# Kernel optimization log

Measured on AMD Instinct MI355X. Metric: run time of the kernel, lower is better.

Reference implementation:

```python
import jax, jax.numpy as jnp
import numpy as np

IN_F = 4096
OUT_F = 11008
GROUP_SIZE = 128
NUM_GROUPS = (IN_F + GROUP_SIZE - 1) // GROUP_SIZE  # 32
N_HIGH = int(OUT_F * 0.25)   # 2752
N_LOW = OUT_F - N_HIGH       # 8256
B, S = 2, 2048


def setup_inputs() -> dict:
    key = jax.random.key(0)
    ks = jax.random.split(key, 9)
    x = jax.random.normal(ks[0], (B, S, IN_F), dtype=jnp.float32)
    # INT8 symmetric codes for high-precision columns
    high_prec_weight = jax.random.randint(ks[1], (IN_F, N_HIGH), -128, 128, dtype=jnp.int32)
    # per-group, per-column scales (positive, realistic magnitude)
    high_prec_scales = jax.random.uniform(ks[2], (NUM_GROUPS, N_HIGH), jnp.float32, 1e-4, 2e-2)
    # 4-bit asymmetric codes in [0, 15]
    low_prec_weight = jax.random.randint(ks[3], (IN_F, N_LOW), 0, 16, dtype=jnp.int32)
    low_prec_scales = jax.random.uniform(ks[4], (IN_F, 1), jnp.float32, 1e-4, 2e-2)
    low_prec_scales2 = jax.random.uniform(ks[5], (1, N_LOW), jnp.float32, 0.5, 2.0)
    low_prec_zeros = jnp.round(jax.random.uniform(ks[6], (IN_F, 1), jnp.float32, 0.0, 15.0))
    # inverse column permutation restoring original order
    col_indices_inv = jax.random.permutation(ks[7], OUT_F).astype(jnp.int64)
    bias = jax.random.normal(ks[8], (OUT_F,), dtype=jnp.float32) * 0.02
    return {
        "x": x,
        "high_prec_weight": high_prec_weight,
        "high_prec_scales": high_prec_scales,
        "low_prec_weight": low_prec_weight,
        "low_prec_scales": low_prec_scales,
        "low_prec_scales2": low_prec_scales2,
        "low_prec_zeros": low_prec_zeros,
        "col_indices_inv": col_indices_inv,
        "bias": bias,
    }


def _dequantize(high_w, high_scales, low_w, low_s1, low_s2, low_z, col_inv):
    # High: group-wise symmetric INT8 dequant. K divisible by GROUP_SIZE here (no pad).
    w_high = (high_w.astype(jnp.float32)
              .reshape(NUM_GROUPS, GROUP_SIZE, N_HIGH)
              * high_scales[:, None, :]).reshape(IN_F, N_HIGH)
    # Low: SINQ dual-scale asymmetric dequant: ((q - z) * s1) * s2
    w_low = (low_w.astype(jnp.float32) - low_z) * low_s1 * low_s2
    # Reassemble original column order: W_kn [in_features, out_features]
    w = jnp.concatenate([w_high, w_low], axis=1)[:, col_inv]
    return w


def reference(x, high_prec_weight, high_prec_scales, low_prec_weight,
              low_prec_scales, low_prec_scales2, low_prec_zeros,
              col_indices_inv, bias):
    w_kn = _dequantize(high_prec_weight, high_prec_scales, low_prec_weight,
                       low_prec_scales, low_prec_scales2, low_prec_zeros,
                       col_indices_inv)
    # F.linear(x, W_original) with W_original = w_kn.T  ->  x @ w_kn
    out = jnp.einsum('bsk,kn->bsn', x, w_kn) + bias
    return out
```

## Files before the change

### kernel.cpp

```cpp
#include <hip/hip_runtime.h>
#include <hip/hip_bf16.h>

#define IN_F   4096
#define OUT_F  11008
#define NHIGH  2752
#define NLOW   8256
#define M_TOT  4096

typedef __attribute__((ext_vector_type(8))) short bf16x8;
typedef __attribute__((ext_vector_type(4))) float f32x4;
typedef __attribute__((ext_vector_type(4))) float f32x4v;

__device__ __forceinline__ short f2bf(float f) {
    union { float f; unsigned u; } v; v.f = f;
    unsigned r = (v.u + 0x7fffu + ((v.u >> 16) & 1u)) >> 16;
    return (short)(r & 0xffffu);
}

__device__ __forceinline__ void async16(const void* g, const void* l) {
    __builtin_amdgcn_global_load_lds(
        (const __attribute__((address_space(1))) unsigned int*)g,
        (__attribute__((address_space(3))) unsigned int*)l, 16, 0, 0);
}

__global__ void fwd_perm_kernel(const int* __restrict__ cinv, int* __restrict__ fwd) {
    int n = blockIdx.x * blockDim.x + threadIdx.x;
    if (n < OUT_F) fwd[cinv[n]] = n;
}

__global__ void cvt_x_kernel(const float* __restrict__ x, short* __restrict__ xb) {
    const int nv = (M_TOT * IN_F) / 8;
    for (int i = blockIdx.x * blockDim.x + threadIdx.x; i < nv;
         i += gridDim.x * blockDim.x) {
        const f32x4v* p = (const f32x4v*)(x + (long)i * 8);
        f32x4v a = __builtin_nontemporal_load(p);
        f32x4v b = __builtin_nontemporal_load(p + 1);
        bf16x8 o;
        o[0] = f2bf(a[0]); o[1] = f2bf(a[1]); o[2] = f2bf(a[2]); o[3] = f2bf(a[3]);
        o[4] = f2bf(b[0]); o[5] = f2bf(b[1]); o[6] = f2bf(b[2]); o[7] = f2bf(b[3]);
        *(bf16x8*)(xb + (long)i * 8) = o;
    }
}

__global__ void dequant_kernel(const int* __restrict__ hw, const float* __restrict__ hs,
                               const int* __restrict__ lw, const float* __restrict__ s1,
                               const float* __restrict__ s2, const float* __restrict__ zp,
                               const int* __restrict__ fwd,
                               short* __restrict__ wt) {
    __shared__ short tile[64 * 66];
    const int t  = threadIdx.x;
    const int c0 = blockIdx.x * 64;
    const int k0 = blockIdx.y * 64;
    const int cl = t & 63;
    const int w  = t >> 6;

    if (c0 < NHIGH) {
        const int ci = c0 + cl;
        #pragma unroll
        for (int i = 0; i < 16; ++i) {
            const int kl = w + 4 * i;
            const int k  = k0 + kl;
            int   q   = __builtin_nontemporal_load(&hw[(long)k * NHIGH + ci]);
            float val = (float)q * hs[(k >> 7) * NHIGH + ci];
            tile[cl * 66 + kl] = f2bf(val);
        }
    } else {
        const int ci = c0 - NHIGH + cl;
        const float s2v = s2[ci];
        #pragma unroll
        for (int i = 0; i < 16; ++i) {
            const int kl = w + 4 * i;
            const int k  = k0 + kl;
            int   q   = __builtin_nontemporal_load(&lw[(long)k * NLOW + ci]);
            float val = ((float)q - zp[k]) * s1[k] * s2v;
            tile[cl * 66 + kl] = f2bf(val);
        }
    }
    __syncthreads();
    const int oc = t >> 2;
    const int kq = (t & 3) * 16;
    bf16x8 o0, o1;
    #pragma unroll
    for (int j = 0; j < 8; ++j) {
        o0[j] = tile[oc * 66 + kq + j];
        o1[j] = tile[oc * 66 + kq + 8 + j];
    }
    const int ndst = fwd[c0 + oc];
    short* dst = wt + (long)ndst * IN_F + k0 + kq;
    *(bf16x8*)dst       = o0;
    *(bf16x8*)(dst + 8) = o1;
}

#define BM 256
#define BN 256
#define BK 64
#define KT (IN_F / BK)
#define NTIL (OUT_F / BN)
#define MTIL (M_TOT / BM)
#define NWG2 (NTIL * MTIL)

#define BAR()    __builtin_amdgcn_s_barrier()
#define VMC0()   asm volatile("s_waitcnt vmcnt(0)" ::: "memory")

__global__ __launch_bounds__(512, 2) void gemm_kernel(
    const short* __restrict__ A,
    const short* __restrict__ Bt,
    const float* __restrict__ bias,
    float* __restrict__ C) {
    __shared__ __align__(16) short lds_s[65536];
    char* const lds = (char*)lds_s;

    const int t    = threadIdx.x;
    const int lane = t & 63;
    const int w    = t >> 6;
    const int wr   = w >> 2;
    const int wc   = w & 3;

    const int swz   = (blockIdx.x % 8) * (NWG2 / 8) + blockIdx.x / 8;
    const int sr    = swz / (4 * NTIL);
    const int in_sr = swz % (4 * NTIL);
    const int nb    = in_sr / 4;
    const int mb    = sr * 4 + (in_sr & 3);
    const int m0    = mb * BM;
    const int n0    = nb * BN;

    const int srow = w * 8 + (lane >> 3);
    const int scb  = ((lane & 7) ^ (lane >> 3)) * 16;
    const char* gA0 = (const char*)A  + (long)(m0 + srow) * (IN_F * 2) + scb;
    const char* gB0 = (const char*)Bt + (long)(n0 + srow) * (IN_F * 2) + scb;

    const int rl  = (lane & 15) * 128;
    const int kb0 = ((lane >> 4) * 16) ^ ((lane & 7) << 4);
    const int kb1 = kb0 ^ 64;

#define STAGE(gbase, region_off, h, ktile) do {                                  \
        const char* _g = (gbase) + (long)((h) * 128) * (IN_F * 2) + (ktile) * 128; \
        char* _l = lds + (region_off) + (h) * 16384 + w * 1024;                  \
        async16(_g,                        _l);                                  \
        async16(_g + (long)64 * (IN_F * 2), _l + 8192);                          \
    } while (0)

    f32x4 acc[8][4];
    #pragma unroll
    for (int i = 0; i < 8; ++i)
        #pragma unroll
        for (int j = 0; j < 4; ++j)
            acc[i][j] = (f32x4){0.f, 0.f, 0.f, 0.f};

    bf16x8 aA[4][2], aB[4][2], b0[2][2], b1[2][2];

#define RD_A(buf, mq, areg) do {                                                 \
        char* _p = lds + (buf) * 65536 + wr * 16384 + (mq) * 8192 + rl;          \
        _Pragma("unroll")                                                        \
        for (int _j = 0; _j < 4; ++_j) {                                         \
            areg[_j][0] = *(const bf16x8*)(_p + _j * 2048 + kb0);                \
            areg[_j][1] = *(const bf16x8*)(_p + _j * 2048 + kb1);                \
        }                                                                        \
    } while (0)

#define RD_B(buf, nq, breg) do {                                                 \
        char* _p = lds + (buf) * 65536 + 32768 + wc * 8192 + (nq) * 4096 + rl;   \
        _Pragma("unroll")                                                        \
        for (int _n = 0; _n < 2; ++_n) {                                         \
            breg[_n][0] = *(const bf16x8*)(_p + _n * 2048 + kb0);                \
            breg[_n][1] = *(const bf16x8*)(_p + _n * 2048 + kb1);                \
        }                                                                        \
    } while (0)

#define MMA_Q(mq, nq, areg, breg) do {                                           \
        __builtin_amdgcn_s_setprio(1);                                           \
        _Pragma("unroll")                                                        \
        for (int _j = 0; _j < 4; ++_j)                                           \
        _Pragma("unroll")                                                        \
        for (int _n = 0; _n < 2; ++_n) {                                         \
            acc[(mq)*4+_j][(nq)*2+_n] = __builtin_amdgcn_mfma_f32_16x16x32_bf16( \
                areg[_j][0], breg[_n][0], acc[(mq)*4+_j][(nq)*2+_n], 0, 0, 0);   \
            acc[(mq)*4+_j][(nq)*2+_n] = __builtin_amdgcn_mfma_f32_16x16x32_bf16( \
                areg[_j][1], breg[_n][1], acc[(mq)*4+_j][(nq)*2+_n], 0, 0, 0);   \
        }                                                                        \
        __builtin_amdgcn_s_setprio(0);                                           \
    } while (0)

#define TILE_BODY(buf, ktn) do {                                                 \
        RD_A(buf, 0, aA);                                                        \
        RD_B(buf, 0, b0);                                                        \
        RD_B(buf, 1, b1);                                                        \
        RD_A(buf, 1, aB);                                                        \
        STAGE(gA0, ((buf)^1) * 65536,         0, ktn);                           \
        STAGE(gA0, ((buf)^1) * 65536,         1, ktn);                           \
        STAGE(gB0, ((buf)^1) * 65536 + 32768, 0, ktn);                           \
        STAGE(gB0, ((buf)^1) * 65536 + 32768, 1, ktn);                           \
        MMA_Q(0, 0, aA, b0);                                                     \
        MMA_Q(0, 1, aA, b1);                                                     \
        MMA_Q(1, 1, aB, b1);                                                     \
        MMA_Q(1, 0, aB, b0);                                                     \
        VMC0(); BAR();                                                           \
    } while (0)

    STAGE(gA0, 0,     0, 0);
    STAGE(gA0, 0,     1, 0);
    STAGE(gB0, 32768, 0, 0);
    STAGE(gB0, 32768, 1, 0);
    VMC0();
    BAR();

    #pragma unroll 1
    for (int it = 0; it < KT / 2; ++it) {
        const int kt1 = 2 * it + 1;
        const int kt2 = (2 * it + 2 < KT) ? 2 * it + 2 : KT - 1;
        TILE_BODY(0, kt1);
        TILE_BODY(1, kt2);
    }

    const int er = m0 + wr * 128 + (lane >> 4) * 4;
    const int ec = n0 + wc * 64 + (lane & 15);
    #pragma unroll
    for (int ni = 0; ni < 4; ++ni) {
        const float bv = bias[ec + ni * 16];
        #pragma unroll
        for (int mi = 0; mi < 8; ++mi) {
            #pragma unroll
            for (int r = 0; r < 4; ++r) {
                __builtin_nontemporal_store(
                    acc[mi][ni][r] + bv,
                    &C[(long)(er + mi * 16 + r) * OUT_F + ec + ni * 16]);
            }
        }
    }
}

extern "C" void kernel_launch(void* const* d_in, const int* in_sizes, int n_in,
                              void* d_out, int out_size, void* d_ws, size_t ws_size,
                              hipStream_t stream) {
    const float* x    = (const float*)d_in[0];
    const int*   hw   = (const int*)d_in[1];
    const float* hs   = (const float*)d_in[2];
    const int*   lw   = (const int*)d_in[3];
    const float* s1   = (const float*)d_in[4];
    const float* s2   = (const float*)d_in[5];
    const float* zp   = (const float*)d_in[6];
    const int*   cinv = (const int*)d_in[7];
    const float* bias = (const float*)d_in[8];
    float*       out  = (float*)d_out;

    short* wt  = (short*)d_ws;
    short* xb  = (short*)((char*)d_ws + (size_t)OUT_F * IN_F * 2);
    int*   fwd = (int*)((char*)d_ws + (size_t)OUT_F * IN_F * 2
                                    + (size_t)M_TOT * IN_F * 2);

    fwd_perm_kernel<<<(OUT_F + 255) / 256, 256, 0, stream>>>(cinv, fwd);
    cvt_x_kernel<<<2048, 256, 0, stream>>>(x, xb);
    dequant_kernel<<<dim3(OUT_F / 64, IN_F / 64), 256, 0, stream>>>(
        hw, hs, lw, s1, s2, zp, fwd, wt);
    gemm_kernel<<<NWG2, 512, 0, stream>>>(xb, wt, bias, out);
}
```

Measured before the change: 393.3 us.

## Shrink GEMM tile to 128x128 with 4-wave workgroups and simpler schedule

Reduces the GEMM macro tile from 256x256 (8 waves) to 128x128 (4 waves, 64x64 per wave), halving LDS to 64KB and restructuring staging and fragment reads into one pass per k-tile. The aim is more workgroups for better CU load balance and occupancy, and a less fragmented tail (11008/256 is not an integer). It gives up operand reuse, so global and L2 traffic per FLOP doubles, and the interleaved read/MMA schedule becomes a plain read-then-compute sequence.

```diff
diff --git a/kernel.cpp b/kernel.cpp
--- a/kernel.cpp
+++ b/kernel.cpp
@@ -91,40 +91,40 @@
     *(bf16x8*)(dst + 8) = o1;
 }
 
-#define BM 256
-#define BN 256
+#define BM 128
+#define BN 128
 #define BK 64
 #define KT (IN_F / BK)
 #define NTIL (OUT_F / BN)
 #define MTIL (M_TOT / BM)
-#define NWG2 (NTIL * MTIL)
+#define NWG3 (NTIL * MTIL)
 
 #define BAR()    __builtin_amdgcn_s_barrier()
 #define VMC0()   asm volatile("s_waitcnt vmcnt(0)" ::: "memory")
 
-__global__ __launch_bounds__(512, 2) void gemm_kernel(
+__global__ __launch_bounds__(256, 2) void gemm_kernel(
     const short* __restrict__ A,
     const short* __restrict__ Bt,
     const float* __restrict__ bias,
     float* __restrict__ C) {
-    __shared__ __align__(16) short lds_s[65536];
+    __shared__ __align__(16) short lds_s[32768];
     char* const lds = (char*)lds_s;
 
     const int t    = threadIdx.x;
     const int lane = t & 63;
     const int w    = t >> 6;
-    const int wr   = w >> 2;
-    const int wc   = w & 3;
-
-    const int swz   = (blockIdx.x % 8) * (NWG2 / 8) + blockIdx.x / 8;
-    const int sr    = swz / (4 * NTIL);
-    const int in_sr = swz % (4 * NTIL);
-    const int nb    = in_sr / 4;
-    const int mb    = sr * 4 + (in_sr & 3);
+    const int wr   = w >> 1;
+    const int wc   = w & 1;
+
+    const int swz   = (blockIdx.x % 8) * (NWG3 / 8) + blockIdx.x / 8;
+    const int sr    = swz / (8 * NTIL);
+    const int in_sr = swz % (8 * NTIL);
+    const int nb    = in_sr / 8;
+    const int mb    = sr * 8 + (in_sr & 7);
     const int m0    = mb * BM;
     const int n0    = nb * BN;
 
-    const int srow = w * 8 + (lane >> 3);
+    const int srow = w * 32 + (lane >> 3);
     const int scb  = ((lane & 7) ^ (lane >> 3)) * 16;
     const char* gA0 = (const char*)A  + (long)(m0 + srow) * (IN_F * 2) + scb;
     const char* gB0 = (const char*)Bt + (long)(n0 + srow) * (IN_F * 2) + scb;
@@ -133,74 +133,57 @@
     const int kb0 = ((lane >> 4) * 16) ^ ((lane & 7) << 4);
     const int kb1 = kb0 ^ 64;
 
-#define STAGE(gbase, region_off, h, ktile) do {                                  \
-        const char* _g = (gbase) + (long)((h) * 128) * (IN_F * 2) + (ktile) * 128; \
-        char* _l = lds + (region_off) + (h) * 16384 + w * 1024;                  \
-        async16(_g,                        _l);                                  \
-        async16(_g + (long)64 * (IN_F * 2), _l + 8192);                          \
+#define STAGE_TILE(buf, ktile) do {                                              \
+        const char* _ga = gA0 + (ktile) * 128;                                   \
+        const char* _gb = gB0 + (ktile) * 128;                                   \
+        char* _la = lds + (buf) * 32768 +         w * 4096 + (lane) * 16;        \
+        char* _lb = lds + (buf) * 32768 + 16384 + w * 4096 + (lane) * 16;        \
+        _Pragma("unroll")                                                        \
+        for (int _j = 0; _j < 4; ++_j) {                                         \
+            async16(_ga + (long)(_j * 8) * (IN_F * 2), _la + _j * 1024);         \
+            async16(_gb + (long)(_j * 8) * (IN_F * 2), _lb + _j * 1024);         \
+        }                                                                        \
     } while (0)
 
-    f32x4 acc[8][4];
+    f32x4 acc[4][4];
     #pragma unroll
-    for (int i = 0; i < 8; ++i)
+    for (int i = 0; i < 4; ++i)
         #pragma unroll
         for (int j = 0; j < 4; ++j)
             acc[i][j] = (f32x4){0.f, 0.f, 0.f, 0.f};
 
-    bf16x8 aA[4][2], aB[4][2], b0[2][2], b1[2][2];
-
-#define RD_A(buf, mq, areg) do {                                                 \
-        char* _p = lds + (buf) * 65536 + wr * 16384 + (mq) * 8192 + rl;          \
-        _Pragma("unroll")                                                        \
-        for (int _j = 0; _j < 4; ++_j) {                                         \
-            areg[_j][0] = *(const bf16x8*)(_p + _j * 2048 + kb0);                \
-            areg[_j][1] = *(const bf16x8*)(_p + _j * 2048 + kb1);                \
+    bf16x8 af[4][2], bfm[4][2];
+
+#define RD_ALL(buf) do {                                                         \
+        char* _pa = lds + (buf) * 32768 +         (wr * 64) * 128 + rl;          \
+        char* _pb = lds + (buf) * 32768 + 16384 + (wc * 64) * 128 + rl;          \
+        _Pragma("unroll")                                                        \
+        for (int _i = 0; _i < 4; ++_i) {                                         \
+            af[_i][0]  = *(const bf16x8*)(_pa + _i * 2048 + kb0);                \
+            af[_i][1]  = *(const bf16x8*)(_pa + _i * 2048 + kb1);                \
+            bfm[_i][0] = *(const bf16x8*)(_pb + _i * 2048 + kb0);                \
+            bfm[_i][1] = *(const bf16x8*)(_pb + _i * 2048 + kb1);                \
         }                                                                        \
     } while (0)
 
-#define RD_B(buf, nq, breg) do {                                                 \
-        char* _p = lds + (buf) * 65536 + 32768 + wc * 8192 + (nq) * 4096 + rl;   \
-        _Pragma("unroll")                                                        \
-        for (int _n = 0; _n < 2; ++_n) {                                         \
-            breg[_n][0] = *(const bf16x8*)(_p + _n * 2048 + kb0);                \
-            breg[_n][1] = *(const bf16x8*)(_p + _n * 2048 + kb1);                \
-        }                                                                        \
-    } while (0)
-
-#define MMA_Q(mq, nq, areg, breg) do {                                           \
+#define TILE_BODY(buf, ktn) do {                                                 \
+        RD_ALL(buf);                                                             \
+        STAGE_TILE((buf) ^ 1, ktn);                                              \
         __builtin_amdgcn_s_setprio(1);                                           \
         _Pragma("unroll")                                                        \
-        for (int _j = 0; _j < 4; ++_j)                                           \
-        _Pragma("unroll")                                                        \
-        for (int _n = 0; _n < 2; ++_n) {                                         \
-            acc[(mq)*4+_j][(nq)*2+_n] = __builtin_amdgcn_mfma_f32_16x16x32_bf16( \
-                areg[_j][0], breg[_n][0], acc[(mq)*4+_j][(nq)*2+_n], 0, 0, 0);   \
-            acc[(mq)*4+_j][(nq)*2+_n] = __builtin_amdgcn_mfma_f32_16x16x32_bf16( \
-                areg[_j][1], breg[_n][1], acc[(mq)*4+_j][(nq)*2+_n], 0, 0, 0);   \
+        for (int _m = 0; _m < 4; ++_m)                                           \
+        _Pragma("unroll")                                                        \
+        for (int _n = 0; _n < 4; ++_n) {                                         \
+            acc[_m][_n] = __builtin_amdgcn_mfma_f32_16x16x32_bf16(               \
+                af[_m][0], bfm[_n][0], acc[_m][_n], 0, 0, 0);                    \
+            acc[_m][_n] = __builtin_amdgcn_mfma_f32_16x16x32_bf16(               \
+                af[_m][1], bfm[_n][1], acc[_m][_n], 0, 0, 0);                    \
         }                                                                        \
         __builtin_amdgcn_s_setprio(0);                                           \
-    } while (0)
-
-#define TILE_BODY(buf, ktn) do {                                                 \
-        RD_A(buf, 0, aA);                                                        \
-        RD_B(buf, 0, b0);                                                        \
-        RD_B(buf, 1, b1);                                                        \
-        RD_A(buf, 1, aB);                                                        \
-        STAGE(gA0, ((buf)^1) * 65536,         0, ktn);                           \
-        STAGE(gA0, ((buf)^1) * 65536,         1, ktn);                           \
-        STAGE(gB0, ((buf)^1) * 65536 + 32768, 0, ktn);                           \
-        STAGE(gB0, ((buf)^1) * 65536 + 32768, 1, ktn);                           \
-        MMA_Q(0, 0, aA, b0);                                                     \
-        MMA_Q(0, 1, aA, b1);                                                     \
-        MMA_Q(1, 1, aB, b1);                                                     \
-        MMA_Q(1, 0, aB, b0);                                                     \
         VMC0(); BAR();                                                           \
     } while (0)
 
-    STAGE(gA0, 0,     0, 0);
-    STAGE(gA0, 0,     1, 0);
-    STAGE(gB0, 32768, 0, 0);
-    STAGE(gB0, 32768, 1, 0);
+    STAGE_TILE(0, 0);
     VMC0();
     BAR();
 
@@ -212,13 +195,13 @@
         TILE_BODY(1, kt2);
     }
 
-    const int er = m0 + wr * 128 + (lane >> 4) * 4;
+    const int er = m0 + wr * 64 + (lane >> 4) * 4;
     const int ec = n0 + wc * 64 + (lane & 15);
     #pragma unroll
     for (int ni = 0; ni < 4; ++ni) {
         const float bv = bias[ec + ni * 16];
         #pragma unroll
-        for (int mi = 0; mi < 8; ++mi) {
+        for (int mi = 0; mi < 4; ++mi) {
             #pragma unroll
             for (int r = 0; r < 4; ++r) {
                 __builtin_nontemporal_store(
@@ -252,5 +235,5 @@
     cvt_x_kernel<<<2048, 256, 0, stream>>>(x, xb);
     dequant_kernel<<<dim3(OUT_F / 64, IN_F / 64), 256, 0, stream>>>(
         hw, hs, lw, s1, s2, zp, fwd, wt);
-    gemm_kernel<<<NWG2, 512, 0, stream>>>(xb, wt, bias, out);
-}
+    gemm_kernel<<<NWG3, 256, 0, stream>>>(xb, wt, bias, out);
+}
```

New measurement: 416.0 us. 5.8% more time.
